# Performance work log

Measured on AMD Instinct MI355X. Metric: run time of the kernel, lower is better.

## Reference

```python
import jax, jax.numpy as jnp
import numpy as np

B, LATENT, H, OUT, T, L = 4096, 128, 256, 88, 64, 5  # batch, latent, hidden, output(88 keys), seq_len, num_layers


def setup_inputs() -> dict:
    key = jax.random.key(0)
    ks = jax.random.split(key, 8)
    sc = 1.0 / np.sqrt(H)
    n = lambda k, shp, s: (jax.random.normal(k, shp, jnp.float32) * s)
    return {
        "x": jax.random.normal(ks[0], (B, LATENT), jnp.float32),
        "linear_w": n(ks[1], (H, LATENT), 1.0 / np.sqrt(LATENT)),
        "linear_b": jnp.zeros((H,), jnp.float32),
        # PyTorch LSTM layout: [4H, in] with gate order i, f, g, o. Layer-0 input size == H.
        "w_ih": n(ks[2], (L, 4 * H, H), sc),
        "w_hh": n(ks[3], (L, 4 * H, H), sc),
        "b_ih": n(ks[4], (L, 4 * H), sc),
        "b_hh": n(ks[5], (L, 4 * H), sc),
        "out_w": n(ks[6], (OUT, H), sc),
        "out_b": jnp.zeros((OUT,), jnp.float32),
    }


def _lstm_cell(gates, c):
    # gates: [B, 4H] pre-activation, PyTorch order i, f, g, o
    i, f, g, o = jnp.split(gates, 4, axis=-1)
    c_new = jax.nn.sigmoid(f) * c + jax.nn.sigmoid(i) * jnp.tanh(g)
    h_new = jax.nn.sigmoid(o) * jnp.tanh(c_new)
    return h_new, c_new


def _lstm(xp, w_ih, w_hh, b_ih, b_hh):
    # xp: [B, H] latent projection, repeated over T timesteps (constant input).
    bsz = xp.shape[0]
    gx0 = xp @ w_ih[0].T + b_ih[0]  # layer-0 input gates, constant across time [B, 4H]
    h0 = jnp.zeros((L, bsz, H), xp.dtype)
    c0 = jnp.zeros((L, bsz, H), xp.dtype)

    def step(carry, _):
        h, c = carry  # [L, B, H]
        hs, cs = [], []
        layer_in_gates = gx0
        for l in range(L):  # fixed small loop over structurally distinct layers
            if l > 0:
                layer_in_gates = hs[-1] @ w_ih[l].T + b_ih[l]
            gates = layer_in_gates + h[l] @ w_hh[l].T + b_hh[l]
            hl, cl = _lstm_cell(gates, c[l])
            hs.append(hl)
            cs.append(cl)
        return (jnp.stack(hs), jnp.stack(cs)), hs[-1]

    _, ys = jax.lax.scan(step, (h0, c0), None, length=T)  # ys: [T, B, H]
    return ys.transpose(1, 0, 2)  # [B, T, H]


def reference(x, linear_w, linear_b, w_ih, w_hh, b_ih, b_hh, out_w, out_b):
    xp = x @ linear_w.T + linear_b  # [B, H]; unsqueeze+repeat folded into constant gx0
    y = _lstm(xp, w_ih, w_hh, b_ih, b_hh)  # [B, T, H]
    return jax.nn.sigmoid(y @ out_w.T + out_b)  # [B, T, OUT]
```

## Files before the change

kernel.cpp:

```cpp
#include <hip/hip_runtime.h>
#include <hip/hip_bf16.h>
#include <cstdint>

#define B_ 4096
#define H_ 256
#define G_ 1024
#define T_ 64
#define L_ 5

typedef __hip_bfloat16 bf16;
typedef __bf16 bf16x8 __attribute__((ext_vector_type(8)));
typedef float f32x4 __attribute__((ext_vector_type(4)));

#define OFF_WCOMB   0ull
#define OFF_WIH0R   5242880ull
#define OFF_LWT     5767168ull
#define OFF_XB      5832704ull
#define OFF_OBW     6881280ull
#define OFF_BIAS    6930432ull
#define OFF_W1      6950912ull
#define OFF_B0X     7213056ull
#define OFF_GX0     9048064ull
#define OFF_H0      25825280ull
#define OFF_H1      34213888ull
#define OFF_C1      42602496ull
#define OFF_YS      63574016ull
#define OFF_C0      199888896ull
#define TOTAL_WS    220860416ull
#define SLOT_H      2097152ull
#define SLOT_C      4194304ull

__device__ __forceinline__ bf16* h_ptr(char* ws, int l, int p) {
  return (bf16*)(ws + (p ? OFF_H1 : OFF_H0) + (size_t)l * SLOT_H);
}
__device__ __forceinline__ float* c_ptr(char* ws, int l, int p) {
  return (float*)(ws + (p ? OFF_C1 : OFF_C0) + (size_t)l * SLOT_C);
}
__device__ __forceinline__ bf16* ys_ptr(char* ws, int s) {
  return (bf16*)(ws + OFF_YS + (size_t)s * SLOT_H);
}

__device__ __forceinline__ float frcp(float x) { return __builtin_amdgcn_rcpf(x); }
__device__ __forceinline__ float fsig(float x) { return frcp(1.0f + __expf(-x)); }
__device__ __forceinline__ float ftanh(float x) { return 1.0f - 2.0f * frcp(1.0f + __expf(2.0f * x)); }

__device__ __forceinline__ void gload16(const void* g, void* l) {
  __builtin_amdgcn_global_load_lds((const __attribute__((address_space(1))) void*)g,
                                   (__attribute__((address_space(3))) void*)l, 16, 0, 0);
}

__device__ __forceinline__ void stage_tile(char* dst, const bf16* src, long stride, int koff,
                                           int wv, int lane) {
#pragma unroll
  for (int i = 0; i < 4; ++i) {
    int r = 32 * wv + 8 * i + (lane >> 3);
    int cb = ((lane & 7) << 4) ^ ((r & 7) << 4);
    const bf16* g = src + (long)r * stride + koff + (cb >> 1);
    char* ld = dst + (32 * wv + 8 * i) * 128;
    gload16(g, ld);
  }
}

template <int OUTMODE>
__device__ void gemm_core(const bf16* __restrict__ A1, int lda1,
                          const bf16* __restrict__ A2,
                          const bf16* __restrict__ W, int ldw, int K,
                          const float* __restrict__ bias,
                          const float* __restrict__ acc2d,
                          float* __restrict__ outF, bf16* __restrict__ outB, int ldo,
                          const float* __restrict__ cIn, float* __restrict__ cOut,
                          bf16* __restrict__ hOut,
                          int mtile, int ntile, char* smem) {
  const int tid = threadIdx.x;
  const int lane = tid & 63, wv = tid >> 6;
  const int wrow = wv >> 1, wcol = wv & 1;
  const int row0 = mtile * 128;
  const int n0 = ntile * 128;

  char* As = smem;
  char* Bs = smem + 16384;

  f32x4 acc[4][4];
  if (acc2d) {
#pragma unroll
    for (int m = 0; m < 4; m++)
#pragma unroll
      for (int n = 0; n < 4; n++)
#pragma unroll
        for (int r = 0; r < 4; r++) {
          int row = row0 + wrow * 64 + 16 * m + ((lane >> 4) << 2) + r;
          int col = n0 + wcol * 64 + 16 * n + (lane & 15);
          acc[m][n][r] = acc2d[(long)row * G_ + col];
        }
  } else {
#pragma unroll
    for (int n = 0; n < 4; n++) {
      int col = n0 + wcol * 64 + 16 * n + (lane & 15);
      float bv = bias ? bias[col] : 0.0f;
#pragma unroll
      for (int m = 0; m < 4; m++)
#pragma unroll
        for (int r = 0; r < 4; r++) acc[m][n][r] = bv;
    }
  }

  const int nkb = K >> 6;
  for (int kb = 0; kb < nkb; ++kb) {
    if (kb < 4) stage_tile(As, A1 + (long)row0 * lda1, lda1, kb * 64, wv, lane);
    else        stage_tile(As, A2 + (long)row0 * 256,  256,  kb * 64 - 256, wv, lane);
    stage_tile(Bs, W + (long)n0 * ldw, ldw, kb * 64, wv, lane);
    __syncthreads();
#pragma unroll
    for (int ks = 0; ks < 2; ++ks) {
      bf16x8 af[4], bfr[4];
#pragma unroll
      for (int m = 0; m < 4; m++) {
        int r = wrow * 64 + 16 * m + (lane & 15);
        int cb = (ks * 64 + ((lane >> 4) << 4)) ^ ((r & 7) << 4);
        af[m] = *(const bf16x8*)(As + r * 128 + cb);
      }
#pragma unroll
      for (int n = 0; n < 4; n++) {
        int r = wcol * 64 + 16 * n + (lane & 15);
        int cb = (ks * 64 + ((lane >> 4) << 4)) ^ ((r & 7) << 4);
        bfr[n] = *(const bf16x8*)(Bs + r * 128 + cb);
      }
#pragma unroll
      for (int m = 0; m < 4; m++)
#pragma unroll
        for (int n = 0; n < 4; n++)
          acc[m][n] = __builtin_amdgcn_mfma_f32_16x16x32_bf16(af[m], bfr[n], acc[m][n], 0, 0, 0);
    }
    __syncthreads();
  }

  if (OUTMODE == 0 || OUTMODE == 1) {
#pragma unroll
    for (int m = 0; m < 4; m++)
#pragma unroll
      for (int n = 0; n < 4; n++)
#pragma unroll
        for (int r = 0; r < 4; r++) {
          int row = row0 + wrow * 64 + 16 * m + ((lane >> 4) << 2) + r;
          int col = n0 + wcol * 64 + 16 * n + (lane & 15);
          if (OUTMODE == 0) outF[(long)row * ldo + col] = acc[m][n][r];
          else              outB[(long)row * ldo + col] = __float2bfloat16(acc[m][n][r]);
        }
  } else {
#pragma unroll
    for (int h = 0; h < 2; ++h) {
      if (wcol == h) {
#pragma unroll
        for (int m = 0; m < 4; m++)
#pragma unroll
          for (int n = 0; n < 4; n++)
#pragma unroll
            for (int r = 0; r < 4; r++) {
              int rr = wrow * 64 + 16 * m + ((lane >> 4) << 2) + r;
              int cc2 = 16 * n + (lane & 15);
              *(float*)(smem + rr * 256 + ((cc2 << 2) ^ ((rr & 7) << 4))) = acc[m][n][r];
            }
      }
      __syncthreads();
      int j2 = tid & 15;
      int rb = tid >> 4;
#pragma unroll
      for (int i = 0; i < 8; i++) {
        int rr = rb + 16 * i;
        f32x4 g4 = *(const f32x4*)(smem + rr * 256 + ((j2 << 4) ^ ((rr & 7) << 4)));
        int row = row0 + rr;
        int jj = ntile * 32 + 16 * h + j2;
        float cold = cIn ? cIn[(long)row * H_ + jj] : 0.0f;
        float cn = fsig(g4[1]) * cold + fsig(g4[0]) * ftanh(g4[2]);
        float hn = fsig(g4[3]) * ftanh(cn);
        cOut[(long)row * H_ + jj] = cn;
        hOut[(long)row * H_ + jj] = __float2bfloat16(hn);
      }
      if (h == 0) __syncthreads();
    }
  }
}

template <int OUTMODE>
__global__ __launch_bounds__(256, 3) void gemm_generic(const bf16* A1, int lda1,
                                                       const bf16* W, int ldw, int K,
                                                       const float* bias,
                                                       float* outF, bf16* outB, int ldo) {
  __shared__ __align__(16) char smem[32768];
  int mtile = blockIdx.x & 31;
  int ntile = blockIdx.x >> 5;
  gemm_core<OUTMODE>(A1, lda1, A1 , W, ldw, K, bias, nullptr,
                     outF, outB, ldo, nullptr, nullptr, nullptr, mtile, ntile, smem);
}

__global__ __launch_bounds__(256, 3) void lstm_diag(int d, char* __restrict__ ws) {
  __shared__ __align__(16) char smem[32768];
  int l0 = d > 63 ? d - 63 : 0;
  int l = l0 + blockIdx.y;
  int t = d - l;
  int mtile = blockIdx.x & 31;
  int ntile = blockIdx.x >> 5;
  int sp = (t & 1) ^ 1, op = t & 1;
  bool tz = (t == 0);

  const bf16* wc = (const bf16*)(ws + OFF_WCOMB) + (long)l * G_ * 512;
  const bf16* A1; const bf16* A2; int K;
  const float* bias = nullptr; const float* acc2d = nullptr;
  if (l == 0) {
    A1 = h_ptr(ws, 0, sp); A2 = A1;
    K = tz ? 0 : 256;
    acc2d = (const float*)(ws + OFF_GX0);
  } else {
    A1 = h_ptr(ws, l - 1, op);
    A2 = (l == 4) ? ys_ptr(ws, t) : h_ptr(ws, l, sp);
    K = tz ? 256 : 512;
    bias = (const float*)(ws + OFF_BIAS) + l * G_;
  }
  const float* cIn = tz ? nullptr : c_ptr(ws, l, sp);
  float* cOut = c_ptr(ws, l, op);
  bf16* hOut = (l == 4) ? ys_ptr(ws, t + 1) : h_ptr(ws, l, op);

  gemm_core<2>(A1, 256, A2, wc, 512, K, bias, acc2d,
               nullptr, nullptr, 0, cIn, cOut, hOut, mtile, ntile, smem);
}

__global__ __launch_bounds__(256) void proj_kernel(char* __restrict__ ws,
                                                   const float* __restrict__ ob,
                                                   float* __restrict__ out) {
  __shared__ __align__(16) char smem[49152];
  int mtile = blockIdx.x;
  int t = blockIdx.y;
  const bf16* ys = ys_ptr(ws, t + 1);
  const char* obw = (const char*)(ws + OFF_OBW);
  int tid = threadIdx.x, lane = tid & 63, wv = tid >> 6;
#pragma unroll
  for (int i = 0; i < 12; i++) {
    int r = wv * 24 + i * 2 + (lane >> 5);
    int cb = ((lane & 31) << 4) ^ ((r & 7) << 4);
    gload16(obw + r * 512 + cb, smem + (wv * 24 + i * 2) * 512);
  }
  __syncthreads();
  f32x4 acc[2][6];
#pragma unroll
  for (int m = 0; m < 2; m++)
#pragma unroll
    for (int n = 0; n < 6; n++)
#pragma unroll
      for (int r = 0; r < 4; r++) acc[m][n][r] = 0.0f;
  const char* arow = (const char*)(ys + (long)(mtile * 128) * 256);
  for (int kk = 0; kk < 256; kk += 32) {
    bf16x8 af[2], bfr[6];
#pragma unroll
    for (int m = 0; m < 2; m++) {
      int r = wv * 32 + 16 * m + (lane & 15);
      af[m] = *(const bf16x8*)(arow + (long)r * 512 + kk * 2 + ((lane >> 4) << 4));
    }
#pragma unroll
    for (int n = 0; n < 6; n++) {
      int r = 16 * n + (lane & 15);
      int cb = (kk * 2 + ((lane >> 4) << 4)) ^ ((r & 7) << 4);
      bfr[n] = *(const bf16x8*)(smem + r * 512 + cb);
    }
#pragma unroll
    for (int m = 0; m < 2; m++)
#pragma unroll
      for (int n = 0; n < 6; n++)
        acc[m][n] = __builtin_amdgcn_mfma_f32_16x16x32_bf16(af[m], bfr[n], acc[m][n], 0, 0, 0);
  }
#pragma unroll
  for (int m = 0; m < 2; m++)
#pragma unroll
    for (int n = 0; n < 6; n++)
#pragma unroll
      for (int r = 0; r < 4; r++) {
        int row = mtile * 128 + wv * 32 + 16 * m + ((lane >> 4) << 2) + r;
        int o = 16 * n + (lane & 15);
        if (o < 88) {
          float v = acc[m][n][r] + ob[o];
          out[((long)row * T_ + t) * 88 + o] = fsig(v);
        }
      }
}

__global__ void prep_kernel(const float* __restrict__ x, const float* __restrict__ lw,
                            const float* __restrict__ wih, const float* __restrict__ whh,
                            const float* __restrict__ bih, const float* __restrict__ bhh,
                            const float* __restrict__ ow, char* __restrict__ ws) {
  bf16* xb = (bf16*)(ws + OFF_XB);
  bf16* lwt = (bf16*)(ws + OFF_LWT);
  bf16* wcomb = (bf16*)(ws + OFF_WCOMB);
  bf16* wih0r = (bf16*)(ws + OFF_WIH0R);
  bf16* obw = (bf16*)(ws + OFF_OBW);
  float* bias = (float*)(ws + OFF_BIAS);
  const int S0 = 524288, S1 = 32768, S2 = 2621440, S3 = 262144, S4 = 24576, S5 = 5120;
  const int total = S0 + S1 + S2 + S3 + S4 + S5;
  for (int i = blockIdx.x * blockDim.x + threadIdx.x; i < total; i += gridDim.x * blockDim.x) {
    int idx = i;
    if (idx < S0) { xb[idx] = __float2bfloat16(x[idx]); continue; }
    idx -= S0;
    if (idx < S1) {
      int r = idx >> 8, c = idx & 255;
      lwt[idx] = __float2bfloat16(lw[c * 128 + r]); continue;
    }
    idx -= S1;
    if (idx < S2) {
      int l = idx >> 19;
      int rem = idx & 524287;
      int n = rem >> 9;
      int k = rem & 511;
      int row = (n & 3) * 256 + (n >> 2);
      float v;
      if (l == 0) v = (k < 256) ? whh[row * 256 + k] : 0.0f;
      else        v = (k < 256) ? wih[(l * 1024 + row) * 256 + k]
                                : whh[(l * 1024 + row) * 256 + (k - 256)];
      wcomb[idx] = __float2bfloat16(v); continue;
    }
    idx -= S2;
    if (idx < S3) {
      int n = idx >> 8, k = idx & 255;
      int row = (n & 3) * 256 + (n >> 2);
      wih0r[idx] = __float2bfloat16(wih[row * 256 + k]); continue;
    }
    idx -= S3;
    if (idx < S4) {
      int r = idx >> 8, k = idx & 255;
      obw[idx] = __float2bfloat16(r < 88 ? ow[r * 256 + k] : 0.0f); continue;
    }
    idx -= S4;
    {
      int l = idx >> 10, n = idx & 1023;
      int row = (n & 3) * 256 + (n >> 2);
      bias[idx] = bih[l * 1024 + row] + bhh[l * 1024 + row];
    }
  }
}

__global__ void bias_fix_kernel(const float* __restrict__ lb, char* __restrict__ ws) {
  int n = blockIdx.x * blockDim.x + threadIdx.x;
  if (n >= 1024) return;
  const bf16* wih0r = (const bf16*)(ws + OFF_WIH0R) + (long)n * 256;
  const float* biasS = (const float*)(ws + OFF_BIAS);
  float s = biasS[n];
  for (int k = 0; k < 256; ++k) s += __bfloat162float(wih0r[k]) * lb[k];
  ((float*)(ws + OFF_B0X))[n] = s;
}

extern "C" void kernel_launch(void* const* d_in, const int* in_sizes, int n_in,
                              void* d_out, int out_size, void* d_ws, size_t ws_size,
                              hipStream_t stream) {
  const float* x   = (const float*)d_in[0];
  const float* lw  = (const float*)d_in[1];
  const float* lb  = (const float*)d_in[2];
  const float* wih = (const float*)d_in[3];
  const float* whh = (const float*)d_in[4];
  const float* bih = (const float*)d_in[5];
  const float* bhh = (const float*)d_in[6];
  const float* ow  = (const float*)d_in[7];
  const float* ob  = (const float*)d_in[8];
  char* ws = (char*)d_ws;
  float* out = (float*)d_out;

  if (ws_size < TOTAL_WS) return;

  prep_kernel<<<2048, 256, 0, stream>>>(x, lw, wih, whh, bih, bhh, ow, ws);

  gemm_generic<1><<<dim3(8), 256, 0, stream>>>(
      (const bf16*)(ws + OFF_WIH0R), 256, (const bf16*)(ws + OFF_LWT), 256, 256,
      nullptr, nullptr, (bf16*)(ws + OFF_W1), 128);

  bias_fix_kernel<<<4, 256, 0, stream>>>(lb, ws);

  gemm_generic<0><<<dim3(256), 256, 0, stream>>>(
      (const bf16*)(ws + OFF_XB), 128, (const bf16*)(ws + OFF_W1), 128, 128,
      (const float*)(ws + OFF_B0X), (float*)(ws + OFF_GX0), nullptr, 1024);

  for (int d = 0; d < 68; ++d) {
    int lo = d > 63 ? d - 63 : 0;
    int hi = d < 4 ? d : 4;
    int nc = hi - lo + 1;
    lstm_diag<<<dim3(256, nc), 256, 0, stream>>>(d, ws);
  }

  proj_kernel<<<dim3(32, 64), 256, 0, stream>>>(ws, ob, out);
}
```

Measured before the change: 2.578 ms.

## Double-buffer GEMM tiles, recompute layer-0 input gates inline, shuffle-based LSTM epilogue

The GEMM main loop now double-buffers A and B tiles in 64KB of shared memory, so the next k-block's global-to-LDS loads overlap the current MFMAs, and only one barrier is needed per iteration. The precomputed fp32 gx0 buffer is dropped; layer 0 instead recomputes x·W1 as two extra k-blocks inside each step, trading extra MFMA work for not reading a large fp32 accumulator from memory. The LSTM cell epilogue transposes the gate values in registers with lane shuffles instead of going through shared memory with barriers. Doubling LDS use and removing the occupancy hint of 3 blocks per CU may lower occupancy.

```diff
diff --git a/kernel.cpp b/kernel.cpp
--- a/kernel.cpp
+++ b/kernel.cpp
@@ -20,7 +20,6 @@
 #define OFF_BIAS    6930432ull
 #define OFF_W1      6950912ull
 #define OFF_B0X     7213056ull
-#define OFF_GX0     9048064ull
 #define OFF_H0      25825280ull
 #define OFF_H1      34213888ull
 #define OFF_C1      42602496ull
@@ -62,12 +61,12 @@
 }
 
 template <int OUTMODE>
-__device__ void gemm_core(const bf16* __restrict__ A1, int lda1,
-                          const bf16* __restrict__ A2,
-                          const bf16* __restrict__ W, int ldw, int K,
+__device__ void gemm_core(const bf16* __restrict__ A1, long lda1,
+                          const bf16* __restrict__ B1, long ldw1, int nkb1,
+                          const bf16* __restrict__ A2, long lda2,
+                          const bf16* __restrict__ B2, long ldw2, int nkb2,
                           const float* __restrict__ bias,
-                          const float* __restrict__ acc2d,
-                          float* __restrict__ outF, bf16* __restrict__ outB, int ldo,
+                          bf16* __restrict__ outB, int ldo,
                           const float* __restrict__ cIn, float* __restrict__ cOut,
                           bf16* __restrict__ hOut,
                           int mtile, int ntile, char* smem) {
@@ -77,11 +76,58 @@
   const int row0 = mtile * 128;
   const int n0 = ntile * 128;
 
-  char* As = smem;
-  char* Bs = smem + 16384;
+  char* As[2] = { smem,          smem + 16384 };
+  char* Bs[2] = { smem + 32768,  smem + 49152 };
 
   f32x4 acc[4][4];
-  if (acc2d) {
+#pragma unroll
+  for (int n = 0; n < 4; n++) {
+    int col = n0 + wcol * 64 + 16 * n + (lane & 15);
+    float bv = bias ? bias[col] : 0.0f;
+#pragma unroll
+    for (int m = 0; m < 4; m++)
+#pragma unroll
+      for (int r = 0; r < 4; r++) acc[m][n][r] = bv;
+  }
+
+  const int nkb = nkb1 + nkb2;
+  auto stageAB = [&](int kb, int b) {
+    const bf16 *sa, *sb; long la, lb; int ko;
+    if (kb < nkb1) { sa = A1; la = lda1; sb = B1; lb = ldw1; ko = kb * 64; }
+    else           { sa = A2; la = lda2; sb = B2; lb = ldw2; ko = (kb - nkb1) * 64; }
+    stage_tile(As[b], sa + (long)row0 * la, la, ko, wv, lane);
+    stage_tile(Bs[b], sb + (long)n0 * lb, lb, ko, wv, lane);
+  };
+
+  stageAB(0, 0);
+  for (int kb = 0; kb < nkb; ++kb) {
+    __syncthreads();
+    if (kb + 1 < nkb) stageAB(kb + 1, (kb + 1) & 1);
+    char* Ab = As[kb & 1]; char* Bb = Bs[kb & 1];
+#pragma unroll
+    for (int ks = 0; ks < 2; ++ks) {
+      bf16x8 af[4], bfr[4];
+#pragma unroll
+      for (int m = 0; m < 4; m++) {
+        int r = wrow * 64 + 16 * m + (lane & 15);
+        int cb = (ks * 64 + ((lane >> 4) << 4)) ^ ((r & 7) << 4);
+        af[m] = *(const bf16x8*)(Ab + r * 128 + cb);
+      }
+#pragma unroll
+      for (int n = 0; n < 4; n++) {
+        int r = wcol * 64 + 16 * n + (lane & 15);
+        int cb = (ks * 64 + ((lane >> 4) << 4)) ^ ((r & 7) << 4);
+        bfr[n] = *(const bf16x8*)(Bb + r * 128 + cb);
+      }
+#pragma unroll
+      for (int m = 0; m < 4; m++)
+#pragma unroll
+        for (int n = 0; n < 4; n++)
+          acc[m][n] = __builtin_amdgcn_mfma_f32_16x16x32_bf16(af[m], bfr[n], acc[m][n], 0, 0, 0);
+    }
+  }
+
+  if (OUTMODE == 1) {
 #pragma unroll
     for (int m = 0; m < 4; m++)
 #pragma unroll
@@ -90,111 +136,46 @@
         for (int r = 0; r < 4; r++) {
           int row = row0 + wrow * 64 + 16 * m + ((lane >> 4) << 2) + r;
           int col = n0 + wcol * 64 + 16 * n + (lane & 15);
-          acc[m][n][r] = acc2d[(long)row * G_ + col];
+          outB[(long)row * ldo + col] = __float2bfloat16(acc[m][n][r]);
         }
   } else {
 #pragma unroll
-    for (int n = 0; n < 4; n++) {
-      int col = n0 + wcol * 64 + 16 * n + (lane & 15);
-      float bv = bias ? bias[col] : 0.0f;
-#pragma unroll
-      for (int m = 0; m < 4; m++)
-#pragma unroll
-        for (int r = 0; r < 4; r++) acc[m][n][r] = bv;
-    }
-  }
-
-  const int nkb = K >> 6;
-  for (int kb = 0; kb < nkb; ++kb) {
-    if (kb < 4) stage_tile(As, A1 + (long)row0 * lda1, lda1, kb * 64, wv, lane);
-    else        stage_tile(As, A2 + (long)row0 * 256,  256,  kb * 64 - 256, wv, lane);
-    stage_tile(Bs, W + (long)n0 * ldw, ldw, kb * 64, wv, lane);
-    __syncthreads();
-#pragma unroll
-    for (int ks = 0; ks < 2; ++ks) {
-      bf16x8 af[4], bfr[4];
-#pragma unroll
-      for (int m = 0; m < 4; m++) {
-        int r = wrow * 64 + 16 * m + (lane & 15);
-        int cb = (ks * 64 + ((lane >> 4) << 4)) ^ ((r & 7) << 4);
-        af[m] = *(const bf16x8*)(As + r * 128 + cb);
+    for (int m = 0; m < 4; m++)
+#pragma unroll
+      for (int n = 0; n < 4; n++) {
+        f32x4 v = acc[m][n];
+        f32x4 t;
+        t[0] = __shfl_xor(v[0], 2); t[1] = __shfl_xor(v[1], 2);
+        t[2] = __shfl_xor(v[2], 2); t[3] = __shfl_xor(v[3], 2);
+        if ((lane & 2) == 0) { v[2] = t[0]; v[3] = t[1]; }
+        else                 { v[0] = t[2]; v[1] = t[3]; }
+        t[0] = __shfl_xor(v[0], 1); t[1] = __shfl_xor(v[1], 1);
+        t[2] = __shfl_xor(v[2], 1); t[3] = __shfl_xor(v[3], 1);
+        if ((lane & 1) == 0) { v[1] = t[0]; v[3] = t[2]; }
+        else                 { v[0] = t[1]; v[2] = t[3]; }
+        int row = row0 + wrow * 64 + 16 * m + ((lane >> 4) << 2) + (lane & 3);
+        int j   = (n0 >> 2) + wcol * 16 + 4 * n + ((lane >> 2) & 3);
+        float cold = cIn ? cIn[(long)row * H_ + j] : 0.0f;
+        float cn = fsig(v[1]) * cold + fsig(v[0]) * ftanh(v[2]);
+        float hn = fsig(v[3]) * ftanh(cn);
+        cOut[(long)row * H_ + j] = cn;
+        hOut[(long)row * H_ + j] = __float2bfloat16(hn);
       }
-#pragma unroll
-      for (int n = 0; n < 4; n++) {
-        int r = wcol * 64 + 16 * n + (lane & 15);
-        int cb = (ks * 64 + ((lane >> 4) << 4)) ^ ((r & 7) << 4);
-        bfr[n] = *(const bf16x8*)(Bs + r * 128 + cb);
-      }
-#pragma unroll
-      for (int m = 0; m < 4; m++)
-#pragma unroll
-        for (int n = 0; n < 4; n++)
-          acc[m][n] = __builtin_amdgcn_mfma_f32_16x16x32_bf16(af[m], bfr[n], acc[m][n], 0, 0, 0);
-    }
-    __syncthreads();
-  }
-
-  if (OUTMODE == 0 || OUTMODE == 1) {
-#pragma unroll
-    for (int m = 0; m < 4; m++)
-#pragma unroll
-      for (int n = 0; n < 4; n++)
-#pragma unroll
-        for (int r = 0; r < 4; r++) {
-          int row = row0 + wrow * 64 + 16 * m + ((lane >> 4) << 2) + r;
-          int col = n0 + wcol * 64 + 16 * n + (lane & 15);
-          if (OUTMODE == 0) outF[(long)row * ldo + col] = acc[m][n][r];
-          else              outB[(long)row * ldo + col] = __float2bfloat16(acc[m][n][r]);
-        }
-  } else {
-#pragma unroll
-    for (int h = 0; h < 2; ++h) {
-      if (wcol == h) {
-#pragma unroll
-        for (int m = 0; m < 4; m++)
-#pragma unroll
-          for (int n = 0; n < 4; n++)
-#pragma unroll
-            for (int r = 0; r < 4; r++) {
-              int rr = wrow * 64 + 16 * m + ((lane >> 4) << 2) + r;
-              int cc2 = 16 * n + (lane & 15);
-              *(float*)(smem + rr * 256 + ((cc2 << 2) ^ ((rr & 7) << 4))) = acc[m][n][r];
-            }
-      }
-      __syncthreads();
-      int j2 = tid & 15;
-      int rb = tid >> 4;
-#pragma unroll
-      for (int i = 0; i < 8; i++) {
-        int rr = rb + 16 * i;
-        f32x4 g4 = *(const f32x4*)(smem + rr * 256 + ((j2 << 4) ^ ((rr & 7) << 4)));
-        int row = row0 + rr;
-        int jj = ntile * 32 + 16 * h + j2;
-        float cold = cIn ? cIn[(long)row * H_ + jj] : 0.0f;
-        float cn = fsig(g4[1]) * cold + fsig(g4[0]) * ftanh(g4[2]);
-        float hn = fsig(g4[3]) * ftanh(cn);
-        cOut[(long)row * H_ + jj] = cn;
-        hOut[(long)row * H_ + jj] = __float2bfloat16(hn);
-      }
-      if (h == 0) __syncthreads();
-    }
-  }
-}
-
-template <int OUTMODE>
-__global__ __launch_bounds__(256, 3) void gemm_generic(const bf16* A1, int lda1,
-                                                       const bf16* W, int ldw, int K,
-                                                       const float* bias,
-                                                       float* outF, bf16* outB, int ldo) {
-  __shared__ __align__(16) char smem[32768];
+  }
+}
+
+__global__ __launch_bounds__(256) void gemm_bf16out(const bf16* A1, long lda1,
+                                                    const bf16* B1, long ldw1, int nkb1,
+                                                    bf16* outB, int ldo) {
+  __shared__ __align__(16) char smem[65536];
   int mtile = blockIdx.x & 31;
   int ntile = blockIdx.x >> 5;
-  gemm_core<OUTMODE>(A1, lda1, A1 , W, ldw, K, bias, nullptr,
-                     outF, outB, ldo, nullptr, nullptr, nullptr, mtile, ntile, smem);
-}
-
-__global__ __launch_bounds__(256, 3) void lstm_diag(int d, char* __restrict__ ws) {
-  __shared__ __align__(16) char smem[32768];
+  gemm_core<1>(A1, lda1, B1, ldw1, nkb1, nullptr, 0, nullptr, 0, 0,
+               nullptr, outB, ldo, nullptr, nullptr, nullptr, mtile, ntile, smem);
+}
+
+__global__ __launch_bounds__(256) void lstm_diag(int d, char* __restrict__ ws) {
+  __shared__ __align__(16) char smem[65536];
   int l0 = d > 63 ? d - 63 : 0;
   int l = l0 + blockIdx.y;
   int t = d - l;
@@ -203,25 +184,36 @@
   int sp = (t & 1) ^ 1, op = t & 1;
   bool tz = (t == 0);
 
+  const bf16* xb = (const bf16*)(ws + OFF_XB);
+  const bf16* W1 = (const bf16*)(ws + OFF_W1);
   const bf16* wc = (const bf16*)(ws + OFF_WCOMB) + (long)l * G_ * 512;
-  const bf16* A1; const bf16* A2; int K;
-  const float* bias = nullptr; const float* acc2d = nullptr;
+
+  const bf16 *A1, *A2 = nullptr, *B1, *B2 = nullptr;
+  long lda1, lda2 = 0, ldw1, ldw2 = 0;
+  int nkb1, nkb2 = 0;
+  const float* bias;
+
   if (l == 0) {
-    A1 = h_ptr(ws, 0, sp); A2 = A1;
-    K = tz ? 0 : 256;
-    acc2d = (const float*)(ws + OFF_GX0);
+    bias = (const float*)(ws + OFF_B0X);
+    if (tz) { A1 = xb; lda1 = 128; B1 = W1; ldw1 = 128; nkb1 = 2; }
+    else {
+      A1 = h_ptr(ws, 0, sp); lda1 = 256; B1 = wc; ldw1 = 512; nkb1 = 4;
+      A2 = xb; lda2 = 128; B2 = W1; ldw2 = 128; nkb2 = 2;
+    }
   } else {
-    A1 = h_ptr(ws, l - 1, op);
-    A2 = (l == 4) ? ys_ptr(ws, t) : h_ptr(ws, l, sp);
-    K = tz ? 256 : 512;
     bias = (const float*)(ws + OFF_BIAS) + l * G_;
+    A1 = h_ptr(ws, l - 1, op); lda1 = 256; B1 = wc; ldw1 = 512; nkb1 = 4;
+    if (!tz) {
+      A2 = (l == 4) ? ys_ptr(ws, t) : h_ptr(ws, l, sp); lda2 = 256;
+      B2 = wc + 256; ldw2 = 512; nkb2 = 4;
+    }
   }
   const float* cIn = tz ? nullptr : c_ptr(ws, l, sp);
   float* cOut = c_ptr(ws, l, op);
   bf16* hOut = (l == 4) ? ys_ptr(ws, t + 1) : h_ptr(ws, l, op);
 
-  gemm_core<2>(A1, 256, A2, wc, 512, K, bias, acc2d,
-               nullptr, nullptr, 0, cIn, cOut, hOut, mtile, ntile, smem);
+  gemm_core<2>(A1, lda1, B1, ldw1, nkb1, A2, lda2, B2, ldw2, nkb2,
+               bias, nullptr, 0, cIn, cOut, hOut, mtile, ntile, smem);
 }
 
 __global__ __launch_bounds__(256) void proj_kernel(char* __restrict__ ws,
@@ -364,15 +356,11 @@
 
   prep_kernel<<<2048, 256, 0, stream>>>(x, lw, wih, whh, bih, bhh, ow, ws);
 
-  gemm_generic<1><<<dim3(8), 256, 0, stream>>>(
-      (const bf16*)(ws + OFF_WIH0R), 256, (const bf16*)(ws + OFF_LWT), 256, 256,
-      nullptr, nullptr, (bf16*)(ws + OFF_W1), 128);
+  gemm_bf16out<<<dim3(8), 256, 0, stream>>>(
+      (const bf16*)(ws + OFF_WIH0R), 256, (const bf16*)(ws + OFF_LWT), 256, 4,
+      (bf16*)(ws + OFF_W1), 128);
 
   bias_fix_kernel<<<4, 256, 0, stream>>>(lb, ws);
-
-  gemm_generic<0><<<dim3(256), 256, 0, stream>>>(
-      (const bf16*)(ws + OFF_XB), 128, (const bf16*)(ws + OFF_W1), 128, 128,
-      (const float*)(ws + OFF_B0X), (float*)(ws + OFF_GX0), nullptr, 1024);
 
   for (int d = 0; d < 68; ++d) {
     int lo = d > 63 ? d - 63 : 0;
```

Measured after the change: 3.177 ms. 23.2% more time.
